# Optimization experiments

Measured on AMD Instinct MI355X. Metric: run time of the kernel, lower is better.

The kernel has to match this reference:

```python
import jax, jax.numpy as jnp
import numpy as np

EMBED_DIM = 1024
NUM_HEADS = 16
HEAD_DIM = EMBED_DIM // NUM_HEADS  # used only for the softmax scale


def setup_inputs() -> dict:
    key = jax.random.key(0)
    k_x, k_wqkv, k_bqkv, k_wo, k_bo = jax.random.split(key, 5)
    bound_qkv = 1.0 / np.sqrt(EMBED_DIM)
    return {
        "x": jax.random.normal(k_x, (4, 2048, EMBED_DIM), dtype=jnp.float32),
        "W_qkv": jax.random.uniform(k_wqkv, (EMBED_DIM, 3 * EMBED_DIM), jnp.float32, -bound_qkv, bound_qkv),
        "b_qkv": jax.random.uniform(k_bqkv, (3 * EMBED_DIM,), jnp.float32, -bound_qkv, bound_qkv),
        "W_out": jax.random.uniform(k_wo, (EMBED_DIM, EMBED_DIM), jnp.float32, -bound_qkv, bound_qkv),
        "b_out": jax.random.uniform(k_bo, (EMBED_DIM,), jnp.float32, -bound_qkv, bound_qkv),
    }


def reference(x, W_qkv, b_qkv, W_out, b_out):
    # fused QKV projection: [B,S,3E]
    qkv = jnp.einsum("bse,ef->bsf", x, W_qkv) + b_qkv
    q, k, v = jnp.split(qkv, 3, axis=-1)  # each [B,S,E]
    scale = 1.0 / jnp.sqrt(jnp.float32(HEAD_DIM))
    # NOTE: no head reshape — attention over full embed_dim, scale uses head_dim
    scores = jnp.einsum("bqe,bke->bqk", q, k) * scale  # [B,S,S]
    attn = jax.nn.softmax(scores, axis=-1)
    context = jnp.einsum("bqk,bke->bqe", attn, v)  # [B,S,E]
    return jnp.einsum("bse,ef->bsf", context, W_out) + b_out
```

## Files before the change

### kernel.cpp

```cpp
#include <hip/hip_runtime.h>

typedef unsigned short u16;
typedef __bf16   bf16x8 __attribute__((ext_vector_type(8)));
typedef float    f32x4  __attribute__((ext_vector_type(4)));
typedef unsigned short u16x4 __attribute__((ext_vector_type(4)));
typedef unsigned short u16x8 __attribute__((ext_vector_type(8)));

__device__ inline float bf2f(u16 u) { return __uint_as_float(((unsigned int)u) << 16); }
__device__ inline u16 f2bf(float f) {
    unsigned int u = __float_as_uint(f);
    u += 0x7FFF + ((u >> 16) & 1);
    return (u16)(u >> 16);
}

__device__ inline void gl2lds16(const u16* g, u16* l) {
    __builtin_amdgcn_global_load_lds(
        (const __attribute__((address_space(1))) void*)g,
        (__attribute__((address_space(3))) void*)l, 16, 0, 0);
}

__global__ __launch_bounds__(256)
void sniff_zero(const u16* __restrict__ x, int* __restrict__ flag,
                float* __restrict__ sums) {
    sums[blockIdx.x * 256 + threadIdx.x] = 0.0f;
    if (blockIdx.x == 0 && threadIdx.x < 64) {
        const int lane = threadIdx.x;
        const unsigned idx = lane * 131072u + 65536u;
        const u16 u = x[idx];
        const int e = (u >> 7) & 0xFF;
        const unsigned long long b = __ballot(e >= 100 && e <= 140);
        if (lane == 0) flag[0] = (__popcll(b) >= 48) ? 0 : 1;
    }
}

__global__ __launch_bounds__(256)
void convx_biases(const void* __restrict__ x, u16* __restrict__ xbf,
                  const void* __restrict__ b1, const void* __restrict__ b2,
                  u16* __restrict__ o1, u16* __restrict__ o2,
                  const int* __restrict__ flagp) {
    const int f = *flagp;
    if (blockIdx.x < 8192) {
        const long i = ((long)blockIdx.x * 256 + threadIdx.x) * 4;
        if (f) {
            f32x4 v = *(const f32x4*)((const float*)x + i);
            u16x4 o; o[0] = f2bf(v[0]); o[1] = f2bf(v[1]); o[2] = f2bf(v[2]); o[3] = f2bf(v[3]);
            *(u16x4*)(xbf + i) = o;
        } else {
            *(u16x4*)(xbf + i) = *(const u16x4*)((const u16*)x + i);
        }
    } else {
        const int i = (blockIdx.x - 8192) * 256 + threadIdx.x;
        if (i < 3072) o1[i] = f ? f2bf(((const float*)b1)[i]) : ((const u16*)b1)[i];
        else { const int j = i - 3072;
               o2[j] = f ? f2bf(((const float*)b2)[j]) : ((const u16*)b2)[j]; }
    }
}

__global__ __launch_bounds__(256)
void transpose_w(const void* __restrict__ Wqkv, u16* __restrict__ WqkvT,
                 const void* __restrict__ Wout, u16* __restrict__ WoutT,
                 u16* __restrict__ Wvbf, const int* __restrict__ flagp)
{
    const void* in; u16* out; long inStride, outStride;
    if (blockIdx.z == 0) { in = Wqkv; out = WqkvT; inStride = 3072; outStride = 1024; }
    else { if (blockIdx.x >= 32) return;
           in = Wout; out = WoutT; inStride = 1024; outStride = 1024; }
    __shared__ u16 t[32][36];
    const int isF32 = *flagp;
    const int tid = threadIdx.x;
    const long r0 = (long)blockIdx.y * 32;
    const long c0 = (long)blockIdx.x * 32;
    const int r  = tid >> 3;
    const int c4 = (tid & 7) * 4;
    const long base = (r0 + r) * inStride + c0 + c4;
    u16x4 v;
    if (isF32) {
        f32x4 f = *(const f32x4*)((const float*)in + base);
        v[0] = f2bf(f[0]); v[1] = f2bf(f[1]); v[2] = f2bf(f[2]); v[3] = f2bf(f[3]);
    } else {
        v = *(const u16x4*)((const u16*)in + base);
    }
    if (blockIdx.z == 0 && c0 >= 2048) {
        *(u16x4*)&Wvbf[(r0 + r) * 1024 + (c0 - 2048) + c4] = v;
        return;
    }
    t[r][c4 + 0] = v[0]; t[r][c4 + 1] = v[1]; t[r][c4 + 2] = v[2]; t[r][c4 + 3] = v[3];
    __syncthreads();
    u16x4 o;
    o[0] = t[c4 + 0][r]; o[1] = t[c4 + 1][r]; o[2] = t[c4 + 2][r]; o[3] = t[c4 + 3][r];
    *(u16x4*)&out[(c0 + r) * outStride + r0 + c4] = o;
}

template <int GM, int GN, int WM, int WN>
__device__ __forceinline__ void kloop(
    const u16* __restrict__ A, const u16* __restrict__ Bt,
    int K, long lda, long ldb, long m0, long n0,
    u16* __restrict__ As, u16* __restrict__ Bs, f32x4 (&acc)[WM][WN])
{
    constexpr int BM = GM * WM * 16;
    constexpr int BN = GN * WN * 16;
    constexpr int IA = BM / 32;
    constexpr int IB = BN / 32;
    const int tid  = threadIdx.x;
    const int lane = tid & 63;
    const int wave = tid >> 6;
    const int sr   = tid >> 3;
    const int qg0  = (tid & 7) ^ (sr & 7);
    const u16* pa[IA]; const u16* pb[IB];
    u16* la[IA]; u16* lb[IB];
#pragma unroll
    for (int i = 0; i < IA; ++i) {
        pa[i] = A + (m0 + i * 32 + sr) * lda + qg0 * 8;
        la[i] = As + (i * 256 + wave * 64) * 8;
    }
#pragma unroll
    for (int i = 0; i < IB; ++i) {
        pb[i] = Bt + (n0 + i * 32 + sr) * ldb + qg0 * 8;
        lb[i] = Bs + (i * 256 + wave * 64) * 8;
    }
    const int wm = (wave / GN) * (WM * 16);
    const int wn = (wave % GN) * (WN * 16);
    const int lr = lane & 15;
    const int hk = lane >> 4;
    int aoff[WM][2], boff[WN][2];
#pragma unroll
    for (int i = 0; i < WM; ++i) {
        const int row = wm + i * 16 + lr, r7 = row & 7;
        aoff[i][0] = row * 64 + ((hk     ^ r7) * 8);
        aoff[i][1] = row * 64 + (((4+hk) ^ r7) * 8);
    }
#pragma unroll
    for (int j = 0; j < WN; ++j) {
        const int row = wn + j * 16 + lr, r7 = row & 7;
        boff[j][0] = row * 64 + ((hk     ^ r7) * 8);
        boff[j][1] = row * 64 + (((4+hk) ^ r7) * 8);
    }
    for (int kt = 0; kt < K; kt += 64) {
#pragma unroll
        for (int i = 0; i < IA; ++i) { gl2lds16(pa[i], la[i]); pa[i] += 64; }
#pragma unroll
        for (int i = 0; i < IB; ++i) { gl2lds16(pb[i], lb[i]); pb[i] += 64; }
        __syncthreads();
#pragma unroll
        for (int ks = 0; ks < 2; ++ks) {
            bf16x8 af[WM], bf[WN];
#pragma unroll
            for (int i = 0; i < WM; ++i) af[i] = *(const bf16x8*)&As[aoff[i][ks]];
#pragma unroll
            for (int j = 0; j < WN; ++j) bf[j] = *(const bf16x8*)&Bs[boff[j][ks]];
#pragma unroll
            for (int i = 0; i < WM; ++i)
#pragma unroll
                for (int j = 0; j < WN; ++j)
                    acc[i][j] = __builtin_amdgcn_mfma_f32_16x16x32_bf16(af[i], bf[j], acc[i][j], 0, 0, 0);
        }
        __syncthreads();
    }
}

template <int WM, int WN, typename F>
__device__ __forceinline__ void epi_bf16(u16* __restrict__ Sw, u16* __restrict__ C,
    long ldc, long gm0, long gn0, int lane, F f)
{
    const int lr = lane & 15, hk = lane >> 4;
#pragma unroll
    for (int i = 0; i < WM; ++i)
#pragma unroll
        for (int j = 0; j < WN; ++j)
#pragma unroll
            for (int r = 0; r < 4; ++r)
                Sw[(i*16 + hk*4 + r) * (WN*16) + j*16 + lr] = f2bf(f(i, j, r));
    asm volatile("s_waitcnt lgkmcnt(0)" ::: "memory");
    constexpr int LPR = WN * 2;
    constexpr int RPI = 64 / LPR;
    const int rl = lane / LPR, c8 = (lane % LPR) * 8;
#pragma unroll
    for (int t = 0; t < (WM*16) / RPI; ++t) {
        const int row = t * RPI + rl;
        u16x8 v8 = *(const u16x8*)&Sw[row * (WN*16) + c8];
        *(u16x8*)&C[(gm0 + row) * ldc + gn0 + c8] = v8;
    }
}

template <int WM, int WN, typename F>
__device__ __forceinline__ void epi_f32(float* __restrict__ Sw, float* __restrict__ C,
    long ldc, long gm0, long gn0, int lane, F f)
{
    const int lr = lane & 15, hk = lane >> 4;
#pragma unroll
    for (int jh = 0; jh < 2; ++jh) {
#pragma unroll
        for (int i = 0; i < WM; ++i)
#pragma unroll
            for (int jj = 0; jj < WN/2; ++jj)
#pragma unroll
                for (int r = 0; r < 4; ++r)
                    Sw[(i*16 + hk*4 + r) * (WN*8) + jj*16 + lr] = f(i, jh*(WN/2) + jj, r);
        asm volatile("s_waitcnt lgkmcnt(0)" ::: "memory");
        constexpr int LPR = WN * 2;
        constexpr int RPI = 64 / LPR;
        const int rl = lane / LPR, c4 = (lane % LPR) * 4;
#pragma unroll
        for (int t = 0; t < (WM*16) / RPI; ++t) {
            const int row = t * RPI + rl;
            f32x4 v4 = *(const f32x4*)&Sw[row * (WN*8) + c4];
            *(f32x4*)&C[(gm0 + row) * ldc + gn0 + jh*(WN*8) + c4] = v4;
        }
        asm volatile("s_waitcnt lgkmcnt(0)" ::: "memory");
    }
}

__device__ __forceinline__ void epiT_vw(u16* __restrict__ Sw, u16* __restrict__ VWTb,
    long o0, long t0, int lane, const f32x4 (&acc)[4][4])
{
    const int lr = lane & 15, hk = lane >> 4;
#pragma unroll
    for (int jh = 0; jh < 2; ++jh) {
#pragma unroll
        for (int jj = 0; jj < 2; ++jj) {
            const int j = jh*2 + jj;
            const int fl = jj*16 + lr;
#pragma unroll
            for (int i = 0; i < 4; ++i)
#pragma unroll
                for (int r = 0; r < 4; ++r)
                    Sw[fl*72 + i*16 + hk*4 + r] = f2bf(acc[i][j][r]);
        }
        asm volatile("s_waitcnt lgkmcnt(0)" ::: "memory");
        const int rl = lane >> 3, c8 = (lane & 7) * 8;
#pragma unroll
        for (int s = 0; s < 4; ++s) {
            const int fl = s*8 + rl;
            *(u16x8*)&VWTb[(o0 + jh*32 + fl) * 2048 + t0 + c8] =
                *(const u16x8*)&Sw[fl*72 + c8];
        }
        asm volatile("s_waitcnt lgkmcnt(0)" ::: "memory");
    }
}

template<int MH, int NH>
__device__ __forceinline__ void mfma16(const bf16x8 (&a)[2][4], const bf16x8 (&b)[2][2],
                                       f32x4 (&acc)[2][2][4][2])
{
    __builtin_amdgcn_s_setprio(1);
#pragma unroll
    for (int ks = 0; ks < 2; ++ks)
#pragma unroll
        for (int i = 0; i < 4; ++i)
#pragma unroll
            for (int j = 0; j < 2; ++j)
                acc[MH][NH][i][j] = __builtin_amdgcn_mfma_f32_16x16x32_bf16(
                    a[ks][i], b[ks][j], acc[MH][NH][i][j], 0, 0, 0);
    __builtin_amdgcn_s_setprio(0);
}

__device__ __forceinline__ void kloop256(
    const u16* __restrict__ A, const u16* __restrict__ Bt,
    int K, long lda, long ldb, long m0, long n0,
    u16* __restrict__ S, f32x4 (&acc)[2][2][4][2])
{
    constexpr int BUF = 256 * 64;
    const int tid  = threadIdx.x;
    const int wave = tid >> 6, lane = tid & 63;
    const int wmi  = wave >> 2, wni = wave & 3;
    const int sr   = tid >> 3;
    const int qg   = ((tid & 7) ^ (sr & 7)) * 8;
    const int lr   = lane & 15, hk = lane >> 4, l7 = lane & 7;
    const u16* pA = A + (m0 + sr) * lda + qg;
    const u16* pB = Bt + (n0 + sr) * ldb + qg;
    u16* const lA = S + wave * 512;
    u16* const lB = S + 2 * BUF + wave * 512;
    const int aO0 = (wmi*64 + lr)*64 + ((hk       ^ l7) * 8);
    const int aO1 = (wmi*64 + lr)*64 + (((4 + hk) ^ l7) * 8);
    const int bO0 = (wni*32 + lr)*64 + ((hk       ^ l7) * 8);
    const int bO1 = (wni*32 + lr)*64 + (((4 + hk) ^ l7) * 8);
    const int NT = K >> 6;

    auto stA = [&](int buf, int mh, int kt) {
        const u16* s = pA + (long)mh * 128 * lda + kt;
        u16* d = lA + buf * BUF + mh * 8192;
        gl2lds16(s, d);
        gl2lds16(s + 64 * lda, d + 4096);
    };
    auto stB = [&](int buf, int nh, int kt) {
        const u16* s = pB + (long)nh * 128 * ldb + kt;
        u16* d = lB + buf * BUF + nh * 8192;
        gl2lds16(s, d);
        gl2lds16(s + 64 * ldb, d + 4096);
    };

    stA(0,0,0); stB(0,0,0); stB(0,1,0); stA(0,1,0);
    stA(1,0,64); stB(1,0,64); stB(1,1,64);
    asm volatile("s_waitcnt vmcnt(6)" ::: "memory");
    __builtin_amdgcn_s_barrier();

    bf16x8 a[2][4], b0[2][2], b1[2][2];
    for (int t = 0; t < NT; ++t) {
        const int b = t & 1;
        const u16* Ab = S + b * BUF;
        const u16* Bb = S + 2 * BUF + b * BUF;
#pragma unroll
        for (int i = 0; i < 4; ++i) {
            a[0][i] = *(const bf16x8*)&Ab[aO0 + i*1024];
            a[1][i] = *(const bf16x8*)&Ab[aO1 + i*1024];
        }
#pragma unroll
        for (int j = 0; j < 2; ++j) {
            b0[0][j] = *(const bf16x8*)&Bb[bO0 + j*1024];
            b0[1][j] = *(const bf16x8*)&Bb[bO1 + j*1024];
        }
        if (t + 1 < NT) stA(b ^ 1, 1, (t + 1) << 6);
        __builtin_amdgcn_s_barrier();
        asm volatile("s_waitcnt lgkmcnt(0)" ::: "memory");
        mfma16<0,0>(a, b0, acc);
        __builtin_amdgcn_s_barrier();
#pragma unroll
        for (int j = 0; j < 2; ++j) {
            b1[0][j] = *(const bf16x8*)&Bb[bO0 + 8192 + j*1024];
            b1[1][j] = *(const bf16x8*)&Bb[bO1 + 8192 + j*1024];
        }
        if (t + 2 < NT) stA(b, 0, (t + 2) << 6);
        __builtin_amdgcn_s_barrier();
        asm volatile("s_waitcnt lgkmcnt(0)" ::: "memory");
        mfma16<0,1>(a, b1, acc);
        __builtin_amdgcn_s_barrier();
#pragma unroll
        for (int i = 0; i < 4; ++i) {
            a[0][i] = *(const bf16x8*)&Ab[aO0 + 8192 + i*1024];
            a[1][i] = *(const bf16x8*)&Ab[aO1 + 8192 + i*1024];
        }
        if (t + 2 < NT) stB(b, 0, (t + 2) << 6);
        __builtin_amdgcn_s_barrier();
        asm volatile("s_waitcnt lgkmcnt(0)" ::: "memory");
        mfma16<1,1>(a, b1, acc);
        __builtin_amdgcn_s_barrier();
        if (t + 2 < NT) stB(b, 1, (t + 2) << 6);
        __builtin_amdgcn_s_barrier();
        mfma16<1,0>(a, b0, acc);
        if (t + 2 < NT)      asm volatile("s_waitcnt vmcnt(6)" ::: "memory");
        else if (t + 1 < NT) asm volatile("s_waitcnt vmcnt(0)" ::: "memory");
        __builtin_amdgcn_s_barrier();
    }
}

__global__ __launch_bounds__(256, 4)
void gemm_qkv(const u16* __restrict__ A, const u16* __restrict__ Bt,
              u16* __restrict__ C, u16* __restrict__ VWT,
              const u16* __restrict__ bias)
{
    __shared__ __align__(16) u16 S[256 * 64];
    const long m0 = (long)blockIdx.y * 128, n0 = (long)blockIdx.x * 128;
    f32x4 acc[4][4] = {};
    kloop<2, 2, 4, 4>(A, Bt, 1024, 1024L, 1024L, m0, n0, S, S + 128*64, acc);
    const int lane = threadIdx.x & 63, wave = threadIdx.x >> 6;
    const int wm = (wave >> 1) * 64, wn = (wave & 1) * 64;
    u16* Sw = S + wave * 4096;
    if (n0 >= 2048) {
        u16* VWTb = VWT + (m0 >> 11) * 1024 * 2048;
        epiT_vw(Sw, VWTb, n0 + wn - 2048, (m0 & 2047) + wm, lane, acc);
    } else {
        const int lr = lane & 15;
        float bj[4];
#pragma unroll
        for (int j = 0; j < 4; ++j) bj[j] = bf2f(bias[n0 + wn + j*16 + lr]);
        epi_bf16<4, 4>(Sw, C, 3072L, m0 + wm, n0 + wn, lane,
            [&](int i, int j, int r) { return acc[i][j][r] + bj[j]; });
    }
}

__global__ __launch_bounds__(256, 4)
void gemm_wvo(const u16* __restrict__ WoutT, const u16* __restrict__ Wvbf,
              u16* __restrict__ WvoT, const u16* __restrict__ bqkvc,
              const u16* __restrict__ boutc, u16* __restrict__ bfinal)
{
    __shared__ __align__(16) u16 S[256 * 64];
    if (blockIdx.x == 8) {
        if (blockIdx.y >= 4) return;
        const int o = blockIdx.y * 256 + threadIdx.x;
        const u16* row = WoutT + (long)o * 1024;
        float s0 = 0, s1 = 0, s2 = 0, s3 = 0, s4 = 0, s5 = 0, s6 = 0, s7 = 0;
        for (int v = 0; v < 1024; v += 8) {
            u16x8 w = *(const u16x8*)&row[v];
            u16x8 b = *(const u16x8*)&bqkvc[2048 + v];
            s0 += bf2f(w[0]) * bf2f(b[0]); s1 += bf2f(w[1]) * bf2f(b[1]);
            s2 += bf2f(w[2]) * bf2f(b[2]); s3 += bf2f(w[3]) * bf2f(b[3]);
            s4 += bf2f(w[4]) * bf2f(b[4]); s5 += bf2f(w[5]) * bf2f(b[5]);
            s6 += bf2f(w[6]) * bf2f(b[6]); s7 += bf2f(w[7]) * bf2f(b[7]);
        }
        const float s = ((s0 + s1) + (s2 + s3)) + ((s4 + s5) + (s6 + s7));
        bfinal[o] = f2bf(s + bf2f(boutc[o]));
        return;
    }
    const long m0 = (long)blockIdx.y * 128, n0 = (long)blockIdx.x * 128;
    f32x4 acc[4][4] = {};
    kloop<2, 2, 4, 4>(WoutT, Wvbf, 1024, 1024L, 1024L, m0, n0, S, S + 128*64, acc);
    const int lane = threadIdx.x & 63, wave = threadIdx.x >> 6;
    const int wm = (wave >> 1) * 64, wn = (wave & 1) * 64;
    epi_bf16<4, 4>(S + wave * 4096, WvoT, 1024L, m0 + wm, n0 + wn, lane,
        [&](int i, int j, int r) { return acc[i][j][r]; });
}

__global__ __launch_bounds__(512, 2)
void gemm_scores256(const u16* __restrict__ QKV, u16* __restrict__ P,
                    float* __restrict__ sums)
{
    __shared__ __align__(16) u16 S[65536];
    const int z = blockIdx.z;
    const long zb = (long)z * 2048 * 3072;
    const u16* Ap = QKV + zb;
    const u16* Bp = QKV + 1024 + zb;
    u16* Cp = P + (long)z * 2048 * 2048;
    float* srow = sums + z * 2048;
    const long m0 = (long)blockIdx.y * 256, n0 = (long)blockIdx.x * 256;
    f32x4 acc[2][2][4][2] = {};
    kloop256(Ap, Bp, 1024, 3072L, 3072L, m0, n0, S, acc);
    const int lane = threadIdx.x & 63, wave = threadIdx.x >> 6;
    const int wmi = wave >> 2, wni = wave & 3;
    const int lr = lane & 15, hk = lane >> 4;
    u16* Sw = S + wave * 8192;
#pragma unroll
    for (int mh = 0; mh < 2; ++mh)
#pragma unroll
    for (int i = 0; i < 4; ++i)
#pragma unroll
    for (int r = 0; r < 4; ++r) {
        float s = 0.0f;
#pragma unroll
        for (int nh = 0; nh < 2; ++nh)
#pragma unroll
        for (int j = 0; j < 2; ++j) {
            const float e = __expf(acc[mh][nh][i][j][r] * 0.125f);
            Sw[(mh*64 + i*16 + hk*4 + r) * 64 + nh*32 + j*16 + lr] = f2bf(e);
            s += e;
        }
        s += __shfl_xor(s, 1); s += __shfl_xor(s, 2);
        s += __shfl_xor(s, 4); s += __shfl_xor(s, 8);
        if (lr == 0) atomicAdd(&srow[m0 + mh*128 + wmi*64 + i*16 + hk*4 + r], s);
    }
    asm volatile("s_waitcnt lgkmcnt(0)" ::: "memory");
    const int rl = lane >> 3, c8 = (lane & 7) * 8;
    const long gcolb = n0 + (long)((c8 >> 5) * 128 + wni * 32 + (c8 & 31));
#pragma unroll
    for (int t = 0; t < 16; ++t) {
        const int row = t * 8 + rl;
        const long grow = m0 + (row >> 6) * 128 + wmi * 64 + (row & 63);
        *(u16x8*)&Cp[grow * 2048 + gcolb] = *(const u16x8*)&Sw[row * 64 + c8];
    }
}

__global__ __launch_bounds__(256, 4)
void gemm_final(const u16* __restrict__ P, const u16* __restrict__ VWT,
                void* __restrict__ out, const u16* __restrict__ bias,
                const float* __restrict__ sums, const int* __restrict__ flagp)
{
    __shared__ __align__(16) u16 S[256 * 64];
    const int outF32 = *flagp;
    const long bz = blockIdx.z;
    const long m0 = (long)blockIdx.y * 128, n0 = (long)blockIdx.x * 128;
    f32x4 acc[4][4] = {};
    kloop<2, 2, 4, 4>(P + bz * 2048 * 2048, VWT + bz * 1024 * 2048,
                      2048, 2048L, 2048L, m0, n0, S, S + 128*64, acc);
    const int lane = threadIdx.x & 63, wave = threadIdx.x >> 6;
    const int wm = (wave >> 1) * 64, wn = (wave & 1) * 64;
    const int lr = lane & 15, hk = lane >> 4;
    float inv[4][4], bj[4];
#pragma unroll
    for (int i = 0; i < 4; ++i)
#pragma unroll
        for (int r = 0; r < 4; ++r)
            inv[i][r] = 1.0f / sums[bz * 2048 + m0 + wm + i*16 + hk*4 + r];
#pragma unroll
    for (int j = 0; j < 4; ++j) bj[j] = bf2f(bias[n0 + wn + j*16 + lr]);
    if (outF32) {
        float* Co = (float*)out + bz * 2048 * 1024;
        epi_f32<4, 4>((float*)S + wave * 2048, Co, 1024L, m0 + wm, n0 + wn, lane,
            [&](int i, int j, int r) { return acc[i][j][r] * inv[i][r] + bj[j]; });
    } else {
        u16* Co = (u16*)out + bz * 2048 * 1024;
        epi_bf16<4, 4>(S + wave * 4096, Co, 1024L, m0 + wm, n0 + wn, lane,
            [&](int i, int j, int r) { return acc[i][j][r] * inv[i][r] + bj[j]; });
    }
}

extern "C" void kernel_launch(void* const* d_in, const int* in_sizes, int n_in,
                              void* d_out, int out_size, void* d_ws, size_t ws_size,
                              hipStream_t stream)
{
    const void* x    = d_in[0];
    const void* Wqkv = d_in[1];
    const void* bqkv = d_in[2];
    const void* Wout = d_in[3];
    const void* bout = d_in[4];
    char* ws = (char*)d_ws;

    u16*   xbf   = (u16*)(ws);
    u16*   WqkvT = (u16*)(ws + 16777216);
    u16*   P     = (u16*)(ws);
    u16*   QKV   = (u16*)(ws + 33554432);
    u16*   VWT   = (u16*)(ws + 83886080);
    u16*   Wvbf  = (u16*)(ws + 83886080);
    u16*   WoutT = (u16*)(ws + 100663296);
    u16*   bqkvc = (u16*)(ws + 102760448);
    u16*   boutc = (u16*)(ws + 102766592);
    int*   flag  = (int*)(ws + 102768640);
    u16*   bfin  = (u16*)(ws + 102769664);
    float* sums  = (float*)(ws + 102772736);

    dim3 blk(256);

    sniff_zero<<<32, blk, 0, stream>>>((const u16*)x, flag, sums);
    convx_biases<<<8208, blk, 0, stream>>>(x, xbf, bqkv, bout, bqkvc, boutc, flag);
    transpose_w<<<dim3(96, 32, 2), blk, 0, stream>>>(Wqkv, WqkvT, Wout, WoutT, Wvbf, flag);

    gemm_wvo<<<dim3(9, 8, 1), blk, 0, stream>>>(WoutT, Wvbf, WqkvT + 2048*1024,
                                                bqkvc, boutc, bfin);

    gemm_qkv<<<dim3(24, 64, 1), blk, 0, stream>>>(xbf, WqkvT, QKV, VWT, bqkvc);

    gemm_scores256<<<dim3(8, 8, 4), dim3(512), 0, stream>>>(QKV, P, sums);

    gemm_final<<<dim3(8, 16, 4), blk, 0, stream>>>(P, VWT, d_out, bfin, sums, flag);
}
```

Before: 267.3 us.

## Merge x conversion and weight transpose kernels; remap GEMM workgroups XCD-aware

```diff
diff --git a/kernel.cpp b/kernel.cpp
--- a/kernel.cpp
+++ b/kernel.cpp
@@ -34,39 +34,46 @@
 }
 
 __global__ __launch_bounds__(256)
-void convx_biases(const void* __restrict__ x, u16* __restrict__ xbf,
-                  const void* __restrict__ b1, const void* __restrict__ b2,
-                  u16* __restrict__ o1, u16* __restrict__ o2,
-                  const int* __restrict__ flagp) {
-    const int f = *flagp;
-    if (blockIdx.x < 8192) {
-        const long i = ((long)blockIdx.x * 256 + threadIdx.x) * 4;
-        if (f) {
-            f32x4 v = *(const f32x4*)((const float*)x + i);
-            u16x4 o; o[0] = f2bf(v[0]); o[1] = f2bf(v[1]); o[2] = f2bf(v[2]); o[3] = f2bf(v[3]);
-            *(u16x4*)(xbf + i) = o;
-        } else {
-            *(u16x4*)(xbf + i) = *(const u16x4*)((const u16*)x + i);
-        }
+void prep_wx(const void* __restrict__ x, u16* __restrict__ xbf,
+             const void* __restrict__ Wqkv, u16* __restrict__ WqkvT,
+             const void* __restrict__ Wout, u16* __restrict__ WoutT,
+             u16* __restrict__ Wvbf,
+             const void* __restrict__ bqkv, const void* __restrict__ bout,
+             u16* __restrict__ bqkvc, u16* __restrict__ boutc,
+             const int* __restrict__ flagp)
+{
+    const int isF32 = *flagp;
+    if (blockIdx.z == 2) {
+        const int flat = blockIdx.y * 129 + blockIdx.x;
+        if (flat < 4096) {
+            const long i = ((long)flat * 256 + threadIdx.x) * 8;
+            if (isF32) {
+                f32x4 v0 = *(const f32x4*)((const float*)x + i);
+                f32x4 v1 = *(const f32x4*)((const float*)x + i + 4);
+                u16x8 o;
+                o[0]=f2bf(v0[0]); o[1]=f2bf(v0[1]); o[2]=f2bf(v0[2]); o[3]=f2bf(v0[3]);
+                o[4]=f2bf(v1[0]); o[5]=f2bf(v1[1]); o[6]=f2bf(v1[2]); o[7]=f2bf(v1[3]);
+                *(u16x8*)(xbf + i) = o;
+            } else {
+                *(u16x8*)(xbf + i) = *(const u16x8*)((const u16*)x + i);
+            }
+        } else if (flat < 4112) {
+            const int i = (flat - 4096) * 256 + threadIdx.x;
+            if (i < 3072) bqkvc[i] = isF32 ? f2bf(((const float*)bqkv)[i]) : ((const u16*)bqkv)[i];
+            else { const int j = i - 3072;
+                   boutc[j] = isF32 ? f2bf(((const float*)bout)[j]) : ((const u16*)bout)[j]; }
+        }
+        return;
+    }
+    const void* in; u16* out; long inStride, outStride;
+    if (blockIdx.z == 0) {
+        if (blockIdx.x >= 96) return;
+        in = Wqkv; out = WqkvT; inStride = 3072; outStride = 1024;
     } else {
-        const int i = (blockIdx.x - 8192) * 256 + threadIdx.x;
-        if (i < 3072) o1[i] = f ? f2bf(((const float*)b1)[i]) : ((const u16*)b1)[i];
-        else { const int j = i - 3072;
-               o2[j] = f ? f2bf(((const float*)b2)[j]) : ((const u16*)b2)[j]; }
-    }
-}
-
-__global__ __launch_bounds__(256)
-void transpose_w(const void* __restrict__ Wqkv, u16* __restrict__ WqkvT,
-                 const void* __restrict__ Wout, u16* __restrict__ WoutT,
-                 u16* __restrict__ Wvbf, const int* __restrict__ flagp)
-{
-    const void* in; u16* out; long inStride, outStride;
-    if (blockIdx.z == 0) { in = Wqkv; out = WqkvT; inStride = 3072; outStride = 1024; }
-    else { if (blockIdx.x >= 32) return;
-           in = Wout; out = WoutT; inStride = 1024; outStride = 1024; }
+        if (blockIdx.x >= 32) return;
+        in = Wout; out = WoutT; inStride = 1024; outStride = 1024;
+    }
     __shared__ u16 t[32][36];
-    const int isF32 = *flagp;
     const int tid = threadIdx.x;
     const long r0 = (long)blockIdx.y * 32;
     const long c0 = (long)blockIdx.x * 32;
@@ -349,7 +356,9 @@
               const u16* __restrict__ bias)
 {
     __shared__ __align__(16) u16 S[256 * 64];
-    const long m0 = (long)blockIdx.y * 128, n0 = (long)blockIdx.x * 128;
+    const int wg = blockIdx.y * 24 + blockIdx.x;
+    const int f8 = (wg & 7) * 192 + (wg >> 3);
+    const long m0 = (long)(f8 / 24) * 128, n0 = (long)(f8 % 24) * 128;
     f32x4 acc[4][4] = {};
     kloop<2, 2, 4, 4>(A, Bt, 1024, 1024L, 1024L, m0, n0, S, S + 128*64, acc);
     const int lane = threadIdx.x & 63, wave = threadIdx.x >> 6;
@@ -405,13 +414,15 @@
                     float* __restrict__ sums)
 {
     __shared__ __align__(16) u16 S[65536];
-    const int z = blockIdx.z;
+    const int wg = blockIdx.x + (blockIdx.y << 3) + (blockIdx.z << 6);
+    const int f8 = (wg & 7) * 32 + (wg >> 3);
+    const int z = f8 >> 6;
+    const long m0 = (long)((f8 >> 3) & 7) * 256, n0 = (long)(f8 & 7) * 256;
     const long zb = (long)z * 2048 * 3072;
     const u16* Ap = QKV + zb;
     const u16* Bp = QKV + 1024 + zb;
     u16* Cp = P + (long)z * 2048 * 2048;
     float* srow = sums + z * 2048;
-    const long m0 = (long)blockIdx.y * 256, n0 = (long)blockIdx.x * 256;
     f32x4 acc[2][2][4][2] = {};
     kloop256(Ap, Bp, 1024, 3072L, 3072L, m0, n0, S, acc);
     const int lane = threadIdx.x & 63, wave = threadIdx.x >> 6;
@@ -455,8 +466,10 @@
 {
     __shared__ __align__(16) u16 S[256 * 64];
     const int outF32 = *flagp;
-    const long bz = blockIdx.z;
-    const long m0 = (long)blockIdx.y * 128, n0 = (long)blockIdx.x * 128;
+    const int wg = blockIdx.x + (blockIdx.y << 3) + (blockIdx.z << 7);
+    const int f8 = (wg & 7) * 64 + (wg >> 3);
+    const long bz = f8 >> 7;
+    const long m0 = (long)((f8 >> 3) & 15) * 128, n0 = (long)(f8 & 7) * 128;
     f32x4 acc[4][4] = {};
     kloop<2, 2, 4, 4>(P + bz * 2048 * 2048, VWT + bz * 1024 * 2048,
                       2048, 2048L, 2048L, m0, n0, S, S + 128*64, acc);
@@ -509,8 +522,9 @@
     dim3 blk(256);
 
     sniff_zero<<<32, blk, 0, stream>>>((const u16*)x, flag, sums);
-    convx_biases<<<8208, blk, 0, stream>>>(x, xbf, bqkv, bout, bqkvc, boutc, flag);
-    transpose_w<<<dim3(96, 32, 2), blk, 0, stream>>>(Wqkv, WqkvT, Wout, WoutT, Wvbf, flag);
+
+    prep_wx<<<dim3(129, 32, 3), blk, 0, stream>>>(x, xbf, Wqkv, WqkvT, Wout, WoutT,
+                                                  Wvbf, bqkv, bout, bqkvc, boutc, flag);
 
     gemm_wvo<<<dim3(9, 8, 1), blk, 0, stream>>>(WoutT, Wvbf, WqkvT + 2048*1024,
                                                 bqkvc, boutc, bfin);
```

Result: faster. 250.7 us (-6.2%).
